# Performance work log

Measured on AMD Instinct MI355X. Metric: run time of the kernel, lower is better.

Reference implementation:

```python
import jax, jax.numpy as jnp
import numpy as np

NUM_ROI = 200

def mish(x):
    return x * jnp.tanh(jax.nn.softplus(x))

def gcn_conv(x, edge_index, edge_weight, W, b):
    # PyG GCNConv: add self-loops (weight 1), symmetric normalization, aggregate at target (col)
    N = x.shape[0]
    row, col = edge_index[0], edge_index[1]
    loop = jnp.arange(N)
    row = jnp.concatenate([row, loop])
    col = jnp.concatenate([col, loop])
    w = jnp.concatenate([edge_weight, jnp.ones((N,), x.dtype)])
    deg = jax.ops.segment_sum(w, col, num_segments=N)
    dis = jnp.where(deg > 0, jax.lax.rsqrt(deg), 0.0)
    norm = dis[row] * w * dis[col]                       # [E+N]
    h = x @ W                                            # [N, out]
    out = jax.ops.segment_sum(h[row] * norm[:, None], col, num_segments=N)
    return out + b

def setup_inputs() -> dict:
    key = jax.random.key(0)
    ks = jax.random.split(key, 16)
    B, E = 256, 1638400
    N = B * NUM_ROI
    d = {}
    d['x'] = jax.random.normal(ks[0], (N, NUM_ROI), jnp.float32)
    d['edge_index'] = jax.random.randint(ks[1], (2, E), 0, N, jnp.int64)
    d['edge_attr'] = jax.random.uniform(ks[2], (E,), jnp.float32)
    def rn(k, shape, fan_in):
        return jax.random.normal(k, shape, jnp.float32) * (1.0 / np.sqrt(fan_in))
    d['W1'] = rn(ks[3], (NUM_ROI, 128), NUM_ROI); d['b1'] = jnp.zeros((128,), jnp.float32)
    d['W2'] = rn(ks[4], (128, 64), 128);          d['b2'] = jnp.zeros((64,), jnp.float32)
    d['Wro'] = rn(ks[5], (64, 8), 64);            d['bro'] = jnp.zeros((8,), jnp.float32)
    d['Wfc1'] = rn(ks[6], (8 * NUM_ROI, NUM_ROI), 8 * NUM_ROI); d['bfc1'] = jnp.zeros((NUM_ROI,), jnp.float32)
    d['bn_gamma'] = jnp.ones((NUM_ROI,), jnp.float32)
    d['bn_beta'] = jnp.zeros((NUM_ROI,), jnp.float32)
    d['Wfc2'] = rn(ks[7], (NUM_ROI, 2), NUM_ROI); d['bfc2'] = jnp.zeros((2,), jnp.float32)
    d['Wd1'] = rn(ks[8], (NUM_ROI, 64), NUM_ROI); d['bd1'] = jnp.zeros((64,), jnp.float32)
    d['Wd2'] = rn(ks[9], (64, 6), 64);            d['bd2'] = jnp.zeros((6,), jnp.float32)
    return d

def reference(x, edge_index, edge_attr, W1, b1, W2, b2, Wro, bro, Wfc1, bfc1,
              bn_gamma, bn_beta, Wfc2, bfc2, Wd1, bd1, Wd2, bd2):
    h = mish(gcn_conv(x, edge_index, edge_attr, W1, b1))
    h = mish(gcn_conv(h, edge_index, edge_attr, W2, b2))
    out = mish(h @ Wro + bro)                            # [N, 8]
    feat = out.reshape(-1, NUM_ROI * 8)                  # [B, 1600]
    z = feat @ Wfc1 + bfc1                               # [B, numROI]
    # BatchNorm1d in training mode (batch statistics, biased variance)
    mu = jnp.mean(z, axis=0)
    var = jnp.mean((z - mu) ** 2, axis=0)
    zn = (z - mu) * jax.lax.rsqrt(var + 1e-5) * bn_gamma + bn_beta
    mid = mish(zn)
    logits = mid @ Wfc2 + bfc2                           # [B, 2]
    rev = 2.0 * jax.lax.stop_gradient(mid) - mid
    cls_logits = jax.nn.relu(rev @ Wd1 + bd1) @ Wd2 + bd2  # [B, 6]
    return (logits, cls_logits)
```

## Files before the change

### kernel.cpp

```cpp
#include <hip/hip_runtime.h>
#include <hip/hip_bf16.h>

typedef __hip_bfloat16 bf16;
typedef __attribute__((ext_vector_type(8))) short short8;
typedef __attribute__((ext_vector_type(4))) float f32x4;

#define NROI 200

__device__ __forceinline__ float u2f(unsigned short u) {
  return __uint_as_float(((unsigned)u) << 16);
}
__device__ __forceinline__ float lo16(unsigned u) { return __uint_as_float(u << 16); }
__device__ __forceinline__ float hi16(unsigned u) { return __uint_as_float(u & 0xffff0000u); }
__device__ __forceinline__ float b2f(bf16 v) { return __bfloat162float(v); }
__device__ __forceinline__ unsigned short f2us(float f) {
  union { bf16 b; unsigned short u; } c;
  c.b = __float2bfloat16(f);
  return c.u;
}

__device__ __forceinline__ float mishf(float x) {
  float sp = (x > 20.0f) ? x : log1pf(expf(x));
  return x * tanhf(sp);
}

__global__ __launch_bounds__(256) void detect_kernel(const unsigned short* xu,
                                                     const unsigned* eiw,
                                                     int* flags) {
  int tid = threadIdx.x;
  int sane = 0, zodd = 0;
  for (int i = tid; i < 4096; i += 256) {
    unsigned short u = xu[2 * i];
    unsigned e = (u >> 7) & 0xFF;
    if (u == 0 || (e >= 100 && e <= 134)) sane++;
  }
  for (int i = tid; i < 4096; i += 256) {
    if (eiw[2 * i + 1] == 0) zodd++;
  }
  __shared__ int s1[256], s2[256];
  s1[tid] = sane; s2[tid] = zodd;
  __syncthreads();
  for (int off = 128; off > 0; off >>= 1) {
    if (tid < off) { s1[tid] += s1[tid + off]; s2[tid] += s2[tid + off]; }
    __syncthreads();
  }
  if (tid == 0) {
    flags[0] = (s1[0] < 2048) ? 1 : 0;
    flags[1] = (s2[0] > 2048) ? 1 : 0;
  }
}

struct WArgs {
  const void* src[16];
  int n[16];
  int off[16];
};

__global__ __launch_bounds__(256) void convert_weights(WArgs a, bf16* base,
                                                       const int* flags) {
  int t = blockIdx.y;
  int i = blockIdx.x * 256 + threadIdx.x;
  if (i >= a.n[t]) return;
  bf16* dst = base + a.off[t];
  if (flags[0]) dst[i] = __float2bfloat16(((const float*)a.src[t])[i]);
  else ((unsigned short*)dst)[i] = ((const unsigned short*)a.src[t])[i];
}

__global__ __launch_bounds__(256) void swizzleW(const unsigned short* __restrict__ src,
                                                unsigned short* __restrict__ dst,
                                                int K, int KC, int NT) {
  int idx = blockIdx.x * 256 + threadIdx.x;
  int total = KC * NT * 512;
  if (idx >= total) return;
  int e = idx & 7;
  int l = (idx >> 3) & 63;
  int t = (idx >> 9) % NT;
  int kc = idx / (NT * 512);
  int k = kc * 32 + (l >> 4) * 8 + e;
  int c = t * 16 + (l & 15);
  dst[idx] = (k < K) ? src[k * (NT * 16) + c] : 0;
}

__global__ __launch_bounds__(256) void xbf_convert(const void* __restrict__ x,
                                                   unsigned short* __restrict__ xb,
                                                   const int* __restrict__ flags,
                                                   int N) {
  long long idx = (long long)blockIdx.x * 256 + threadIdx.x;
  long long total = (long long)N * 224;
  if (idx >= total) return;
  int c = (int)(idx % 224);
  long long n = idx / 224;
  unsigned short v = 0;
  if (c < 200) {
    if (flags[0]) v = f2us(((const float*)x)[n * 200 + c]);
    else v = ((const unsigned short*)x)[n * 200 + c];
  }
  xb[idx] = v;
}


__global__ void init_dc8(unsigned long long* dc8, long long M) {
  long long i = (long long)blockIdx.x * blockDim.x + threadIdx.x;
  if (i < M) dc8[i] = 0ull;
}

__global__ void edge_count(const int* __restrict__ ei, const void* __restrict__ ea,
                           const int* __restrict__ flags,
                           unsigned long long* dc8, int* __restrict__ rank,
                           int N, int E) {
  int e = blockIdx.x * blockDim.x + threadIdx.x;
  if (e >= E) return;
  unsigned xcd;
  asm("s_getreg_b32 %0, hwreg(HW_REG_XCC_ID)" : "=s"(xcd));
  xcd &= 7;
  int is64 = flags[1], isf32 = flags[0];
  int col = is64 ? ei[2 * (E + e)] : ei[E + e];
  float w = isf32 ? ((const float*)ea)[e] : u2f(((const unsigned short*)ea)[e]);
  unsigned long long p = (1ull << 40) | (unsigned long long)(w * 4294967296.0f);
  unsigned long long old = __hip_atomic_fetch_add(&dc8[(size_t)xcd * N + col], p,
                                                  __ATOMIC_RELAXED,
                                                  __HIP_MEMORY_SCOPE_WORKGROUP);
  rank[e] = ((int)xcd << 20) | (int)(old >> 40);
}

__global__ __launch_bounds__(256) void xcd_base(const unsigned long long* __restrict__ dc8,
                                                float* __restrict__ dis,
                                                int* __restrict__ cnt,
                                                unsigned short* __restrict__ xb, int N) {
  int n = blockIdx.x * 256 + threadIdx.x;
  if (n >= N) return;
  int run = 0;
  unsigned long long ws = 0;
  unsigned short loc[8];
#pragma unroll
  for (int x = 0; x < 8; ++x) {
    unsigned long long v = dc8[(size_t)x * N + n];
    loc[x] = (unsigned short)run;
    run += (int)(v >> 40);
    ws += v & 0xFFFFFFFFFFull;
  }
  cnt[n] = run;
  dis[n] = rsqrtf(1.0f + (float)ws * 2.3283064365386963e-10f);
  uint4 o;
  o.x = (unsigned)loc[0] | ((unsigned)loc[1] << 16);
  o.y = (unsigned)loc[2] | ((unsigned)loc[3] << 16);
  o.z = (unsigned)loc[4] | ((unsigned)loc[5] << 16);
  o.w = (unsigned)loc[6] | ((unsigned)loc[7] << 16);
  ((uint4*)xb)[n] = o;
}

__global__ __launch_bounds__(256) void scan_phase1(const int* __restrict__ cnt,
                                                   int* __restrict__ bsum, int N) {
  __shared__ int ts[256];
  int tid = threadIdx.x;
  int base = blockIdx.x * 1024 + tid * 4;
  int s = 0;
#pragma unroll
  for (int j = 0; j < 4; ++j)
    if (base + j < N) s += cnt[base + j];
  ts[tid] = s;
  __syncthreads();
  for (int off = 128; off > 0; off >>= 1) {
    if (tid < off) ts[tid] += ts[tid + off];
    __syncthreads();
  }
  if (tid == 0) bsum[blockIdx.x] = ts[0];
}

__global__ __launch_bounds__(64) void scan_phase2(const int* __restrict__ bsum,
                                                  int* __restrict__ bpre,
                                                  int* __restrict__ ptr, int nb, int N) {
  if (threadIdx.x == 0) {
    int run = 0;
    for (int i = 0; i < nb; ++i) { bpre[i] = run; run += bsum[i]; }
    ptr[N] = run;
  }
}

__global__ __launch_bounds__(256) void scan_phase3(const int* __restrict__ cnt,
                                                   const int* __restrict__ bpre,
                                                   int* __restrict__ ptr, int N) {
  __shared__ int ts[256];
  int tid = threadIdx.x;
  int base = blockIdx.x * 1024 + tid * 4;
  int c0 = 0, c1 = 0, c2 = 0, c3 = 0;
  if (base + 0 < N) c0 = cnt[base + 0];
  if (base + 1 < N) c1 = cnt[base + 1];
  if (base + 2 < N) c2 = cnt[base + 2];
  if (base + 3 < N) c3 = cnt[base + 3];
  ts[tid] = c0 + c1 + c2 + c3;
  __syncthreads();
  for (int off = 1; off < 256; off <<= 1) {
    int v = ts[tid];
    if (tid >= off) v += ts[tid - off];
    __syncthreads();
    ts[tid] = v;
    __syncthreads();
  }
  int run = bpre[blockIdx.x] + (tid ? ts[tid - 1] : 0);
  if (base + 0 < N) { ptr[base + 0] = run; run += c0; }
  if (base + 1 < N) { ptr[base + 1] = run; run += c1; }
  if (base + 2 < N) { ptr[base + 2] = run; run += c2; }
  if (base + 3 < N) { ptr[base + 3] = run; run += c3; }
}

__global__ void edge_scatter(const int* __restrict__ ei, const void* __restrict__ ea,
                             const int* __restrict__ flags,
                             const float* __restrict__ dis,
                             const int* __restrict__ ptr,
                             const unsigned short* __restrict__ xb,
                             const int* __restrict__ rank,
                             int2* __restrict__ epair, int E) {
  int e = blockIdx.x * blockDim.x + threadIdx.x;
  if (e >= E) return;
  int is64 = flags[1], isf32 = flags[0];
  int r = is64 ? ei[2 * e] : ei[e];
  int c = is64 ? ei[2 * (E + e)] : ei[E + e];
  float w = isf32 ? ((const float*)ea)[e] : u2f(((const unsigned short*)ea)[e]);
  float nrm = dis[r] * w * dis[c];
  int rk = rank[e];
  int idx = ptr[c] + (int)xb[(size_t)c * 8 + (rk >> 20)] + (rk & 0xFFFFF);
  int2 pr; pr.x = r; pr.y = __float_as_int(nrm);
  epair[idx] = pr;
}

template<int KC, int NT>
__global__ __launch_bounds__(256) void gemm_mfma(const unsigned short* __restrict__ Abf,
                                                 const unsigned short* __restrict__ Wswz,
                                                 unsigned short* __restrict__ H,
                                                 int M) {
  int wid = threadIdx.x >> 6, lane = threadIdx.x & 63;
  int row0 = (blockIdx.x * 4 + wid) * 16;
  if (row0 >= M) return;
  constexpr int K = KC * 32;
  constexpr int NC = NT * 16;
  f32x4 acc[NT];
#pragma unroll
  for (int t = 0; t < NT; ++t) acc[t] = {0.f, 0.f, 0.f, 0.f};
  size_t arow = (size_t)(row0 + (lane & 15)) * K + (lane >> 4) * 8;
#pragma unroll
  for (int kc = 0; kc < KC; ++kc) {
    short8 a = *(const short8*)&Abf[arow + kc * 32];
#pragma unroll
    for (int t = 0; t < NT; ++t) {
      short8 b = *(const short8*)&Wswz[((kc * NT + t) * 64 + lane) * 8];
      acc[t] = __builtin_amdgcn_mfma_f32_16x16x32_bf16(a, b, acc[t], 0, 0, 0);
    }
  }
  int orow = row0 + (lane >> 4) * 4;
  int ocol = lane & 15;
#pragma unroll
  for (int t = 0; t < NT; ++t)
#pragma unroll
    for (int r = 0; r < 4; ++r)
      H[(size_t)(orow + r) * NC + t * 16 + ocol] = f2us(acc[t][r]);
}

__global__ __launch_bounds__(256) void agg_mish128(const unsigned* __restrict__ hu,
                                                   const float* __restrict__ dis,
                                                   const int* __restrict__ ptr,
                                                   const int2* __restrict__ ep,
                                                   const bf16* __restrict__ bias,
                                                   unsigned* __restrict__ g, int N) {
  int w = threadIdx.x >> 6, lane = threadIdx.x & 63;
  int n = blockIdx.x * 4 + w;
  float dn = dis[n];
  float self = dn * dn;
  unsigned u = hu[(size_t)n * 64 + lane];
  float acc0 = lo16(u) * self;
  float acc1 = hi16(u) * self;
  int e0 = ptr[n], e1 = ptr[n + 1];
  for (int base = e0; base < e1; base += 64) {
    int2 myp = {0, 0};
    if (base + lane < e1) myp = ep[base + lane];
    int m = e1 - base; if (m > 64) m = 64;
    int j = 0;
    for (; j + 4 <= m; j += 4) {
      int r0 = __builtin_amdgcn_readlane(myp.x, j);
      int r1 = __builtin_amdgcn_readlane(myp.x, j + 1);
      int r2 = __builtin_amdgcn_readlane(myp.x, j + 2);
      int r3 = __builtin_amdgcn_readlane(myp.x, j + 3);
      unsigned u0 = hu[(size_t)r0 * 64 + lane];
      unsigned u1 = hu[(size_t)r1 * 64 + lane];
      unsigned u2 = hu[(size_t)r2 * 64 + lane];
      unsigned u3 = hu[(size_t)r3 * 64 + lane];
      float w0 = __uint_as_float(__builtin_amdgcn_readlane(myp.y, j));
      float w1 = __uint_as_float(__builtin_amdgcn_readlane(myp.y, j + 1));
      float w2 = __uint_as_float(__builtin_amdgcn_readlane(myp.y, j + 2));
      float w3 = __uint_as_float(__builtin_amdgcn_readlane(myp.y, j + 3));
      acc0 += lo16(u0) * w0; acc1 += hi16(u0) * w0;
      acc0 += lo16(u1) * w1; acc1 += hi16(u1) * w1;
      acc0 += lo16(u2) * w2; acc1 += hi16(u2) * w2;
      acc0 += lo16(u3) * w3; acc1 += hi16(u3) * w3;
    }
    for (; j < m; ++j) {
      int rr = __builtin_amdgcn_readlane(myp.x, j);
      float ww = __uint_as_float(__builtin_amdgcn_readlane(myp.y, j));
      unsigned uu = hu[(size_t)rr * 64 + lane];
      acc0 += lo16(uu) * ww;
      acc1 += hi16(uu) * ww;
    }
  }
  unsigned bb = ((const unsigned*)bias)[lane];
  float m0 = mishf(acc0 + lo16(bb));
  float m1 = mishf(acc1 + hi16(bb));
  g[(size_t)n * 64 + lane] = ((unsigned)f2us(m1) << 16) | f2us(m0);
}

__global__ __launch_bounds__(256) void agg_mish64_ro(const unsigned short* __restrict__ hus,
                                                     const float* __restrict__ dis,
                                                     const int* __restrict__ ptr,
                                                     const int2* __restrict__ ep,
                                                     const bf16* __restrict__ bias,
                                                     const bf16* __restrict__ Wro,
                                                     const bf16* __restrict__ bro,
                                                     float* __restrict__ out8, int N) {
  int w = threadIdx.x >> 6, lane = threadIdx.x & 63;
  int n = blockIdx.x * 4 + w;
  float dn = dis[n];
  float self = dn * dn;
  float acc = u2f(hus[(size_t)n * 64 + lane]) * self;
  int e0 = ptr[n], e1 = ptr[n + 1];
  for (int base = e0; base < e1; base += 64) {
    int2 myp = {0, 0};
    if (base + lane < e1) myp = ep[base + lane];
    int m = e1 - base; if (m > 64) m = 64;
    int j = 0;
    for (; j + 4 <= m; j += 4) {
      int r0 = __builtin_amdgcn_readlane(myp.x, j);
      int r1 = __builtin_amdgcn_readlane(myp.x, j + 1);
      int r2 = __builtin_amdgcn_readlane(myp.x, j + 2);
      int r3 = __builtin_amdgcn_readlane(myp.x, j + 3);
      float v0 = u2f(hus[(size_t)r0 * 64 + lane]);
      float v1 = u2f(hus[(size_t)r1 * 64 + lane]);
      float v2 = u2f(hus[(size_t)r2 * 64 + lane]);
      float v3 = u2f(hus[(size_t)r3 * 64 + lane]);
      float w0 = __uint_as_float(__builtin_amdgcn_readlane(myp.y, j));
      float w1 = __uint_as_float(__builtin_amdgcn_readlane(myp.y, j + 1));
      float w2 = __uint_as_float(__builtin_amdgcn_readlane(myp.y, j + 2));
      float w3 = __uint_as_float(__builtin_amdgcn_readlane(myp.y, j + 3));
      acc += v0 * w0 + v1 * w1 + v2 * w2 + v3 * w3;
    }
    for (; j < m; ++j) {
      int rr = __builtin_amdgcn_readlane(myp.x, j);
      float ww = __uint_as_float(__builtin_amdgcn_readlane(myp.y, j));
      acc += u2f(hus[(size_t)rr * 64 + lane]) * ww;
    }
  }
  float mv = mishf(acc + u2f(((const unsigned short*)bias)[lane]));
  uint4 wr = ((const uint4*)Wro)[lane];
  float p0 = mv * lo16(wr.x), p1 = mv * hi16(wr.x);
  float p2 = mv * lo16(wr.y), p3 = mv * hi16(wr.y);
  float p4 = mv * lo16(wr.z), p5 = mv * hi16(wr.z);
  float p6 = mv * lo16(wr.w), p7 = mv * hi16(wr.w);
  bool b0 = lane & 1;
  float q0 = (b0 ? p4 : p0) + __shfl_xor(b0 ? p0 : p4, 1);
  float q1 = (b0 ? p5 : p1) + __shfl_xor(b0 ? p1 : p5, 1);
  float q2 = (b0 ? p6 : p2) + __shfl_xor(b0 ? p2 : p6, 1);
  float q3 = (b0 ? p7 : p3) + __shfl_xor(b0 ? p3 : p7, 1);
  bool b1 = lane & 2;
  float r0 = (b1 ? q2 : q0) + __shfl_xor(b1 ? q0 : q2, 2);
  float r1 = (b1 ? q3 : q1) + __shfl_xor(b1 ? q1 : q3, 2);
  bool b2v = lane & 4;
  float t = (b2v ? r1 : r0) + __shfl_xor(b2v ? r0 : r1, 4);
  t += __shfl_xor(t, 8);
  t += __shfl_xor(t, 16);
  t += __shfl_xor(t, 32);
  if (lane < 8) {
    int oidx = ((lane & 1) << 2) | (lane & 2) | ((lane >> 2) & 1);
    out8[(size_t)n * 8 + oidx] = mishf(t + u2f(((const unsigned short*)bro)[oidx]));
  }
}


__global__ __launch_bounds__(256) void fc1_kernel(const float* __restrict__ feat,
                                                  const bf16* __restrict__ W,
                                                  const bf16* __restrict__ bias,
                                                  float* __restrict__ z) {
  __shared__ float fr[1600];
  int b = blockIdx.x, tid = threadIdx.x;
  for (int i = tid; i < 1600; i += 256) fr[i] = feat[(size_t)b * 1600 + i];
  __syncthreads();
  if (tid < NROI) {
    float acc = b2f(bias[tid]);
#pragma unroll 8
    for (int k = 0; k < 1600; ++k) acc += fr[k] * b2f(W[k * NROI + tid]);
    z[b * NROI + tid] = acc;
  }
}

__global__ __launch_bounds__(256) void bn_stats(const float* __restrict__ z,
                                                float* mu, float* rvar, int B) {
  int j = blockIdx.x;
  int tid = threadIdx.x;
  float v = z[tid * NROI + j];
  float s = v, q = v * v;
  for (int off = 32; off > 0; off >>= 1) {
    s += __shfl_down(s, off);
    q += __shfl_down(q, off);
  }
  __shared__ float ss[4], qq[4];
  int w = tid >> 6, lane = tid & 63;
  if (lane == 0) { ss[w] = s; qq[w] = q; }
  __syncthreads();
  if (tid == 0) {
    float S = ss[0] + ss[1] + ss[2] + ss[3];
    float Q = qq[0] + qq[1] + qq[2] + qq[3];
    float m = S / (float)B;
    float var = Q / (float)B - m * m;
    mu[j] = m;
    rvar[j] = rsqrtf(var + 1e-5f);
  }
}

__global__ __launch_bounds__(256) void head_kernel(const float* __restrict__ z,
                                                   const float* __restrict__ mu,
                                                   const float* __restrict__ rvar,
                                                   const bf16* __restrict__ gamma,
                                                   const bf16* __restrict__ beta,
                                                   const bf16* __restrict__ Wfc2,
                                                   const bf16* __restrict__ bfc2,
                                                   const bf16* __restrict__ Wd1,
                                                   const bf16* __restrict__ bd1,
                                                   const bf16* __restrict__ Wd2,
                                                   const bf16* __restrict__ bd2,
                                                   float* __restrict__ out, int B) {
  __shared__ float mid[NROI];
  __shared__ float t[64];
  int b = blockIdx.x, tid = threadIdx.x;
  if (tid < NROI) {
    float v = (z[b * NROI + tid] - mu[tid]) * rvar[tid] * b2f(gamma[tid]) + b2f(beta[tid]);
    mid[tid] = mishf(v);
  }
  __syncthreads();
  if (tid < 64) {
    float acc = b2f(bd1[tid]);
#pragma unroll 8
    for (int j = 0; j < NROI; ++j) acc += mid[j] * b2f(Wd1[j * 64 + tid]);
    t[tid] = fmaxf(acc, 0.0f);
  }
  if (tid >= 64 && tid < 66) {
    int c = tid - 64;
    float acc = b2f(bfc2[c]);
    for (int j = 0; j < NROI; ++j) acc += mid[j] * b2f(Wfc2[j * 2 + c]);
    out[b * 2 + c] = acc;
  }
  __syncthreads();
  if (tid < 6) {
    float acc = b2f(bd2[tid]);
#pragma unroll 8
    for (int k = 0; k < 64; ++k) acc += t[k] * b2f(Wd2[k * 6 + tid]);
    out[B * 2 + b * 6 + tid] = acc;
  }
}


extern "C" void kernel_launch(void* const* d_in, const int* in_sizes, int n_in,
                              void* d_out, int out_size, void* d_ws, size_t ws_size,
                              hipStream_t stream) {
  const void* x  = d_in[0];
  const int*  ei = (const int*)d_in[1];
  const void* ea = d_in[2];
  float* out = (float*)d_out;

  int N = in_sizes[0] / NROI;
  int E = in_sizes[2];
  int B = N / NROI;

  char* p = (char*)d_ws;
  auto carve = [&](size_t bytes) -> void* {
    void* r = (void*)p;
    p += (bytes + 255) & ~(size_t)255;
    return r;
  };
  int*   flags = (int*)carve(16);
  bf16*  cw    = (bf16*)carve(400000 * 2);
  float* dis   = (float*)carve((size_t)N * 4);
  unsigned long long* dc8 = (unsigned long long*)carve((size_t)8 * N * 8);
  int*   cnt   = (int*)carve((size_t)N * 4);
  unsigned short* xbse = (unsigned short*)carve((size_t)N * 8 * 2);
  int*   ptr   = (int*)carve(((size_t)N + 1) * 4);
  int*   bsum  = (int*)carve(1024);
  int*   bpre  = (int*)carve(1024);
  int2*  epair = (int2*)carve((size_t)E * 8);
  unsigned short* h = (unsigned short*)carve((size_t)N * 128 * 2);
  size_t xg_bytes = (size_t)N * 224 * 2;
  size_t rk_bytes = (size_t)E * 4;
  char* xg = (char*)carve(xg_bytes > rk_bytes ? xg_bytes : rk_bytes);
  int* rank = (int*)xg;
  unsigned short* xbf = (unsigned short*)xg;
  unsigned* g = (unsigned*)xg;
  unsigned short* w1swz = (unsigned short*)carve(7 * 8 * 512 * 2);
  unsigned short* w2swz = (unsigned short*)carve(4 * 4 * 512 * 2);
  float* out8  = (float*)carve((size_t)N * 8 * 4);
  float* z     = (float*)carve((size_t)B * NROI * 4);
  float* mu    = (float*)carve(NROI * 4);
  float* rv    = (float*)carve(NROI * 4);

  WArgs wa;
  int run = 0;
  int maxn = 0;
  for (int t = 0; t < 16; ++t) {
    wa.src[t] = d_in[3 + t];
    wa.n[t]   = in_sizes[3 + t];
    wa.off[t] = run;
    run += in_sizes[3 + t];
    if (in_sizes[3 + t] > maxn) maxn = in_sizes[3 + t];
  }
  const bf16* W1   = cw + wa.off[0];
  const bf16* b1   = cw + wa.off[1];
  const bf16* W2   = cw + wa.off[2];
  const bf16* b2   = cw + wa.off[3];
  const bf16* Wro  = cw + wa.off[4];
  const bf16* bro  = cw + wa.off[5];
  const bf16* Wfc1 = cw + wa.off[6];
  const bf16* bfc1 = cw + wa.off[7];
  const bf16* gam  = cw + wa.off[8];
  const bf16* bet  = cw + wa.off[9];
  const bf16* Wfc2 = cw + wa.off[10];
  const bf16* bfc2 = cw + wa.off[11];
  const bf16* Wd1  = cw + wa.off[12];
  const bf16* bd1  = cw + wa.off[13];
  const bf16* Wd2  = cw + wa.off[14];
  const bf16* bd2  = cw + wa.off[15];

  int nb = (N + 255) / 256;
  int eb = (E + 255) / 256;
  int nscan = (N + 1023) / 1024;

  detect_kernel<<<1, 256, 0, stream>>>((const unsigned short*)x,
                                       (const unsigned*)ei, flags);
  dim3 wg((maxn + 255) / 256, 16);
  convert_weights<<<wg, 256, 0, stream>>>(wa, cw, flags);
  swizzleW<<<(7 * 8 * 512 + 255) / 256, 256, 0, stream>>>(
      (const unsigned short*)W1, w1swz, 200, 7, 8);
  swizzleW<<<(4 * 4 * 512 + 255) / 256, 256, 0, stream>>>(
      (const unsigned short*)W2, w2swz, 128, 4, 4);

  long long dctot = (long long)8 * N;
  init_dc8<<<(int)((dctot + 255) / 256), 256, 0, stream>>>(dc8, dctot);
  edge_count<<<eb, 256, 0, stream>>>(ei, ea, flags, dc8, rank, N, E);
  xcd_base<<<nb, 256, 0, stream>>>(dc8, dis, cnt, xbse, N);
  scan_phase1<<<nscan, 256, 0, stream>>>(cnt, bsum, N);
  scan_phase2<<<1, 64, 0, stream>>>(bsum, bpre, ptr, nscan, N);
  scan_phase3<<<nscan, 256, 0, stream>>>(cnt, bpre, ptr, N);
  edge_scatter<<<eb, 256, 0, stream>>>(ei, ea, flags, dis, ptr, xbse, rank,
                                       epair, E);

  long long xtot = (long long)N * 224;
  xbf_convert<<<(int)((xtot + 255) / 256), 256, 0, stream>>>(x, xbf, flags, N);
  gemm_mfma<7, 8><<<N / 64, 256, 0, stream>>>(xbf, w1swz, h, N);
  agg_mish128<<<N / 4, 256, 0, stream>>>((const unsigned*)h, dis, ptr, epair,
                                         b1, g, N);
  gemm_mfma<4, 4><<<N / 64, 256, 0, stream>>>((const unsigned short*)g, w2swz, h, N);
  agg_mish64_ro<<<N / 4, 256, 0, stream>>>(h, dis, ptr, epair, b2, Wro, bro,
                                           out8, N);

  fc1_kernel<<<B, 256, 0, stream>>>(out8, Wfc1, bfc1, z);
  bn_stats<<<NROI, 256, 0, stream>>>(z, mu, rv, B);
  head_kernel<<<B, 256, 0, stream>>>(z, mu, rv, gam, bet, Wfc2, bfc2,
                                     Wd1, bd1, Wd2, bd2, out, B);
}
```

Before: 385.8 us.

## Fuse prep and scan kernels, add nontemporal edge-stream accesses

```diff
diff --git a/kernel.cpp b/kernel.cpp
--- a/kernel.cpp
+++ b/kernel.cpp
@@ -66,12 +66,9 @@
   else ((unsigned short*)dst)[i] = ((const unsigned short*)a.src[t])[i];
 }
 
-__global__ __launch_bounds__(256) void swizzleW(const unsigned short* __restrict__ src,
-                                                unsigned short* __restrict__ dst,
-                                                int K, int KC, int NT) {
-  int idx = blockIdx.x * 256 + threadIdx.x;
-  int total = KC * NT * 512;
-  if (idx >= total) return;
+__device__ __forceinline__ void swz_one(const unsigned short* src,
+                                        unsigned short* dst, int idx,
+                                        int K, int NT) {
   int e = idx & 7;
   int l = (idx >> 3) & 63;
   int t = (idx >> 9) % NT;
@@ -81,28 +78,36 @@
   dst[idx] = (k < K) ? src[k * (NT * 16) + c] : 0;
 }
 
-__global__ __launch_bounds__(256) void xbf_convert(const void* __restrict__ x,
-                                                   unsigned short* __restrict__ xb,
+__global__ __launch_bounds__(256) void prep_kernel(const unsigned short* __restrict__ w1,
+                                                   const unsigned short* __restrict__ w2,
+                                                   unsigned short* __restrict__ w1swz,
+                                                   unsigned short* __restrict__ w2swz,
+                                                   const void* __restrict__ x,
+                                                   unsigned short* __restrict__ xbf,
+                                                   unsigned long long* __restrict__ dc8,
                                                    const int* __restrict__ flags,
-                                                   int N) {
-  long long idx = (long long)blockIdx.x * 256 + threadIdx.x;
-  long long total = (long long)N * 224;
-  if (idx >= total) return;
-  int c = (int)(idx % 224);
-  long long n = idx / 224;
-  unsigned short v = 0;
-  if (c < 200) {
-    if (flags[0]) v = f2us(((const float*)x)[n * 200 + c]);
-    else v = ((const unsigned short*)x)[n * 200 + c];
-  }
-  xb[idx] = v;
-}
-
-
-__global__ void init_dc8(unsigned long long* dc8, long long M) {
-  long long i = (long long)blockIdx.x * blockDim.x + threadIdx.x;
-  if (i < M) dc8[i] = 0ull;
-}
+                                                   int N, int b1, int b2, long long b3,
+                                                   long long b4) {
+  long long i = (long long)blockIdx.x * 256 + threadIdx.x;
+  if (i < b1) {
+    swz_one(w1, w1swz, (int)i, 200, 8);
+  } else if (i < b2) {
+    swz_one(w2, w2swz, (int)(i - b1), 128, 4);
+  } else if (i < b3) {
+    long long idx = i - b2;
+    int c = (int)(idx % 224);
+    long long n = idx / 224;
+    unsigned short v = 0;
+    if (c < 200) {
+      if (flags[0]) v = f2us(((const float*)x)[n * 200 + c]);
+      else v = ((const unsigned short*)x)[n * 200 + c];
+    }
+    xbf[idx] = v;
+  } else if (i < b4) {
+    dc8[i - b3] = 0ull;
+  }
+}
+
 
 __global__ void edge_count(const int* __restrict__ ei, const void* __restrict__ ea,
                            const int* __restrict__ flags,
@@ -114,51 +119,46 @@
   asm("s_getreg_b32 %0, hwreg(HW_REG_XCC_ID)" : "=s"(xcd));
   xcd &= 7;
   int is64 = flags[1], isf32 = flags[0];
-  int col = is64 ? ei[2 * (E + e)] : ei[E + e];
-  float w = isf32 ? ((const float*)ea)[e] : u2f(((const unsigned short*)ea)[e]);
+  int col = is64 ? __builtin_nontemporal_load(&ei[2 * (E + e)])
+                 : __builtin_nontemporal_load(&ei[E + e]);
+  float w = isf32 ? __builtin_nontemporal_load(&((const float*)ea)[e])
+                  : u2f(__builtin_nontemporal_load(&((const unsigned short*)ea)[e]));
   unsigned long long p = (1ull << 40) | (unsigned long long)(w * 4294967296.0f);
   unsigned long long old = __hip_atomic_fetch_add(&dc8[(size_t)xcd * N + col], p,
                                                   __ATOMIC_RELAXED,
                                                   __HIP_MEMORY_SCOPE_WORKGROUP);
-  rank[e] = ((int)xcd << 20) | (int)(old >> 40);
+  __builtin_nontemporal_store(((int)xcd << 20) | (int)(old >> 40), &rank[e]);
 }
 
 __global__ __launch_bounds__(256) void xcd_base(const unsigned long long* __restrict__ dc8,
                                                 float* __restrict__ dis,
                                                 int* __restrict__ cnt,
-                                                unsigned short* __restrict__ xb, int N) {
-  int n = blockIdx.x * 256 + threadIdx.x;
-  if (n >= N) return;
-  int run = 0;
-  unsigned long long ws = 0;
-  unsigned short loc[8];
-#pragma unroll
-  for (int x = 0; x < 8; ++x) {
-    unsigned long long v = dc8[(size_t)x * N + n];
-    loc[x] = (unsigned short)run;
-    run += (int)(v >> 40);
-    ws += v & 0xFFFFFFFFFFull;
-  }
-  cnt[n] = run;
-  dis[n] = rsqrtf(1.0f + (float)ws * 2.3283064365386963e-10f);
-  uint4 o;
-  o.x = (unsigned)loc[0] | ((unsigned)loc[1] << 16);
-  o.y = (unsigned)loc[2] | ((unsigned)loc[3] << 16);
-  o.z = (unsigned)loc[4] | ((unsigned)loc[5] << 16);
-  o.w = (unsigned)loc[6] | ((unsigned)loc[7] << 16);
-  ((uint4*)xb)[n] = o;
-}
-
-__global__ __launch_bounds__(256) void scan_phase1(const int* __restrict__ cnt,
-                                                   int* __restrict__ bsum, int N) {
+                                                unsigned short* __restrict__ xb,
+                                                int* __restrict__ bsum, int N) {
   __shared__ int ts[256];
   int tid = threadIdx.x;
-  int base = blockIdx.x * 1024 + tid * 4;
-  int s = 0;
+  int n = blockIdx.x * 256 + tid;
+  int run = 0;
+  if (n < N) {
+    unsigned long long ws = 0;
+    unsigned short loc[8];
 #pragma unroll
-  for (int j = 0; j < 4; ++j)
-    if (base + j < N) s += cnt[base + j];
-  ts[tid] = s;
+    for (int x = 0; x < 8; ++x) {
+      unsigned long long v = dc8[(size_t)x * N + n];
+      loc[x] = (unsigned short)run;
+      run += (int)(v >> 40);
+      ws += v & 0xFFFFFFFFFFull;
+    }
+    cnt[n] = run;
+    dis[n] = rsqrtf(1.0f + (float)ws * 2.3283064365386963e-10f);
+    uint4 o;
+    o.x = (unsigned)loc[0] | ((unsigned)loc[1] << 16);
+    o.y = (unsigned)loc[2] | ((unsigned)loc[3] << 16);
+    o.z = (unsigned)loc[4] | ((unsigned)loc[5] << 16);
+    o.w = (unsigned)loc[6] | ((unsigned)loc[7] << 16);
+    ((uint4*)xb)[n] = o;
+  }
+  ts[tid] = run;
   __syncthreads();
   for (int off = 128; off > 0; off >>= 1) {
     if (tid < off) ts[tid] += ts[tid + off];
@@ -182,13 +182,9 @@
                                                    int* __restrict__ ptr, int N) {
   __shared__ int ts[256];
   int tid = threadIdx.x;
-  int base = blockIdx.x * 1024 + tid * 4;
-  int c0 = 0, c1 = 0, c2 = 0, c3 = 0;
-  if (base + 0 < N) c0 = cnt[base + 0];
-  if (base + 1 < N) c1 = cnt[base + 1];
-  if (base + 2 < N) c2 = cnt[base + 2];
-  if (base + 3 < N) c3 = cnt[base + 3];
-  ts[tid] = c0 + c1 + c2 + c3;
+  int n = blockIdx.x * 256 + tid;
+  int c = (n < N) ? cnt[n] : 0;
+  ts[tid] = c;
   __syncthreads();
   for (int off = 1; off < 256; off <<= 1) {
     int v = ts[tid];
@@ -197,11 +193,7 @@
     ts[tid] = v;
     __syncthreads();
   }
-  int run = bpre[blockIdx.x] + (tid ? ts[tid - 1] : 0);
-  if (base + 0 < N) { ptr[base + 0] = run; run += c0; }
-  if (base + 1 < N) { ptr[base + 1] = run; run += c1; }
-  if (base + 2 < N) { ptr[base + 2] = run; run += c2; }
-  if (base + 3 < N) { ptr[base + 3] = run; run += c3; }
+  if (n < N) ptr[n] = bpre[blockIdx.x] + (tid ? ts[tid - 1] : 0);
 }
 
 __global__ void edge_scatter(const int* __restrict__ ei, const void* __restrict__ ea,
@@ -210,18 +202,22 @@
                              const int* __restrict__ ptr,
                              const unsigned short* __restrict__ xb,
                              const int* __restrict__ rank,
-                             int2* __restrict__ epair, int E) {
+                             long long* __restrict__ epair, int E) {
   int e = blockIdx.x * blockDim.x + threadIdx.x;
   if (e >= E) return;
   int is64 = flags[1], isf32 = flags[0];
-  int r = is64 ? ei[2 * e] : ei[e];
-  int c = is64 ? ei[2 * (E + e)] : ei[E + e];
-  float w = isf32 ? ((const float*)ea)[e] : u2f(((const unsigned short*)ea)[e]);
+  int r = is64 ? __builtin_nontemporal_load(&ei[2 * e])
+               : __builtin_nontemporal_load(&ei[e]);
+  int c = is64 ? __builtin_nontemporal_load(&ei[2 * (E + e)])
+               : __builtin_nontemporal_load(&ei[E + e]);
+  float w = isf32 ? __builtin_nontemporal_load(&((const float*)ea)[e])
+                  : u2f(__builtin_nontemporal_load(&((const unsigned short*)ea)[e]));
   float nrm = dis[r] * w * dis[c];
-  int rk = rank[e];
+  int rk = __builtin_nontemporal_load(&rank[e]);
   int idx = ptr[c] + (int)xb[(size_t)c * 8 + (rk >> 20)] + (rk & 0xFFFFF);
-  int2 pr; pr.x = r; pr.y = __float_as_int(nrm);
-  epair[idx] = pr;
+  long long pr = (long long)((unsigned long long)__float_as_uint(nrm) << 32) |
+                 (unsigned)r;
+  __builtin_nontemporal_store(pr, &epair[idx]);
 }
 
 template<int KC, int NT>
@@ -259,7 +255,7 @@
 __global__ __launch_bounds__(256) void agg_mish128(const unsigned* __restrict__ hu,
                                                    const float* __restrict__ dis,
                                                    const int* __restrict__ ptr,
-                                                   const int2* __restrict__ ep,
+                                                   const long long* __restrict__ ep,
                                                    const bf16* __restrict__ bias,
                                                    unsigned* __restrict__ g, int N) {
   int w = threadIdx.x >> 6, lane = threadIdx.x & 63;
@@ -271,31 +267,33 @@
   float acc1 = hi16(u) * self;
   int e0 = ptr[n], e1 = ptr[n + 1];
   for (int base = e0; base < e1; base += 64) {
-    int2 myp = {0, 0};
-    if (base + lane < e1) myp = ep[base + lane];
+    long long myp = 0;
+    if (base + lane < e1) myp = __builtin_nontemporal_load(&ep[base + lane]);
+    int mx = (int)(unsigned)myp;
+    int my = (int)(myp >> 32);
     int m = e1 - base; if (m > 64) m = 64;
     int j = 0;
     for (; j + 4 <= m; j += 4) {
-      int r0 = __builtin_amdgcn_readlane(myp.x, j);
-      int r1 = __builtin_amdgcn_readlane(myp.x, j + 1);
-      int r2 = __builtin_amdgcn_readlane(myp.x, j + 2);
-      int r3 = __builtin_amdgcn_readlane(myp.x, j + 3);
+      int r0 = __builtin_amdgcn_readlane(mx, j);
+      int r1 = __builtin_amdgcn_readlane(mx, j + 1);
+      int r2 = __builtin_amdgcn_readlane(mx, j + 2);
+      int r3 = __builtin_amdgcn_readlane(mx, j + 3);
       unsigned u0 = hu[(size_t)r0 * 64 + lane];
       unsigned u1 = hu[(size_t)r1 * 64 + lane];
       unsigned u2 = hu[(size_t)r2 * 64 + lane];
       unsigned u3 = hu[(size_t)r3 * 64 + lane];
-      float w0 = __uint_as_float(__builtin_amdgcn_readlane(myp.y, j));
-      float w1 = __uint_as_float(__builtin_amdgcn_readlane(myp.y, j + 1));
-      float w2 = __uint_as_float(__builtin_amdgcn_readlane(myp.y, j + 2));
-      float w3 = __uint_as_float(__builtin_amdgcn_readlane(myp.y, j + 3));
+      float w0 = __uint_as_float(__builtin_amdgcn_readlane(my, j));
+      float w1 = __uint_as_float(__builtin_amdgcn_readlane(my, j + 1));
+      float w2 = __uint_as_float(__builtin_amdgcn_readlane(my, j + 2));
+      float w3 = __uint_as_float(__builtin_amdgcn_readlane(my, j + 3));
       acc0 += lo16(u0) * w0; acc1 += hi16(u0) * w0;
       acc0 += lo16(u1) * w1; acc1 += hi16(u1) * w1;
       acc0 += lo16(u2) * w2; acc1 += hi16(u2) * w2;
       acc0 += lo16(u3) * w3; acc1 += hi16(u3) * w3;
     }
     for (; j < m; ++j) {
-      int rr = __builtin_amdgcn_readlane(myp.x, j);
-      float ww = __uint_as_float(__builtin_amdgcn_readlane(myp.y, j));
+      int rr = __builtin_amdgcn_readlane(mx, j);
+      float ww = __uint_as_float(__builtin_amdgcn_readlane(my, j));
       unsigned uu = hu[(size_t)rr * 64 + lane];
       acc0 += lo16(uu) * ww;
       acc1 += hi16(uu) * ww;
@@ -310,7 +308,7 @@
 __global__ __launch_bounds__(256) void agg_mish64_ro(const unsigned short* __restrict__ hus,
                                                      const float* __restrict__ dis,
                                                      const int* __restrict__ ptr,
-                                                     const int2* __restrict__ ep,
+                                                     const long long* __restrict__ ep,
                                                      const bf16* __restrict__ bias,
                                                      const bf16* __restrict__ Wro,
                                                      const bf16* __restrict__ bro,
@@ -322,28 +320,30 @@
   float acc = u2f(hus[(size_t)n * 64 + lane]) * self;
   int e0 = ptr[n], e1 = ptr[n + 1];
   for (int base = e0; base < e1; base += 64) {
-    int2 myp = {0, 0};
-    if (base + lane < e1) myp = ep[base + lane];
+    long long myp = 0;
+    if (base + lane < e1) myp = __builtin_nontemporal_load(&ep[base + lane]);
+    int mx = (int)(unsigned)myp;
+    int my = (int)(myp >> 32);
     int m = e1 - base; if (m > 64) m = 64;
     int j = 0;
     for (; j + 4 <= m; j += 4) {
-      int r0 = __builtin_amdgcn_readlane(myp.x, j);
-      int r1 = __builtin_amdgcn_readlane(myp.x, j + 1);
-      int r2 = __builtin_amdgcn_readlane(myp.x, j + 2);
-      int r3 = __builtin_amdgcn_readlane(myp.x, j + 3);
+      int r0 = __builtin_amdgcn_readlane(mx, j);
+      int r1 = __builtin_amdgcn_readlane(mx, j + 1);
+      int r2 = __builtin_amdgcn_readlane(mx, j + 2);
+      int r3 = __builtin_amdgcn_readlane(mx, j + 3);
       float v0 = u2f(hus[(size_t)r0 * 64 + lane]);
       float v1 = u2f(hus[(size_t)r1 * 64 + lane]);
       float v2 = u2f(hus[(size_t)r2 * 64 + lane]);
       float v3 = u2f(hus[(size_t)r3 * 64 + lane]);
-      float w0 = __uint_as_float(__builtin_amdgcn_readlane(myp.y, j));
-      float w1 = __uint_as_float(__builtin_amdgcn_readlane(myp.y, j + 1));
-      float w2 = __uint_as_float(__builtin_amdgcn_readlane(myp.y, j + 2));
-      float w3 = __uint_as_float(__builtin_amdgcn_readlane(myp.y, j + 3));
+      float w0 = __uint_as_float(__builtin_amdgcn_readlane(my, j));
+      float w1 = __uint_as_float(__builtin_amdgcn_readlane(my, j + 1));
+      float w2 = __uint_as_float(__builtin_amdgcn_readlane(my, j + 2));
+      float w3 = __uint_as_float(__builtin_amdgcn_readlane(my, j + 3));
       acc += v0 * w0 + v1 * w1 + v2 * w2 + v3 * w3;
     }
     for (; j < m; ++j) {
-      int rr = __builtin_amdgcn_readlane(myp.x, j);
-      float ww = __uint_as_float(__builtin_amdgcn_readlane(myp.y, j));
+      int rr = __builtin_amdgcn_readlane(mx, j);
+      float ww = __uint_as_float(__builtin_amdgcn_readlane(my, j));
       acc += u2f(hus[(size_t)rr * 64 + lane]) * ww;
     }
   }
@@ -482,12 +482,10 @@
   int*   ptr   = (int*)carve(((size_t)N + 1) * 4);
   int*   bsum  = (int*)carve(1024);
   int*   bpre  = (int*)carve(1024);
-  int2*  epair = (int2*)carve((size_t)E * 8);
+  long long* epair = (long long*)carve((size_t)E * 8);
   unsigned short* h = (unsigned short*)carve((size_t)N * 128 * 2);
-  size_t xg_bytes = (size_t)N * 224 * 2;
-  size_t rk_bytes = (size_t)E * 4;
-  char* xg = (char*)carve(xg_bytes > rk_bytes ? xg_bytes : rk_bytes);
-  int* rank = (int*)xg;
+  int*   rank  = (int*)carve((size_t)E * 4);
+  char* xg = (char*)carve((size_t)N * 224 * 2);
   unsigned short* xbf = (unsigned short*)xg;
   unsigned* g = (unsigned*)xg;
   unsigned short* w1swz = (unsigned short*)carve(7 * 8 * 512 * 2);
@@ -526,29 +524,27 @@
 
   int nb = (N + 255) / 256;
   int eb = (E + 255) / 256;
-  int nscan = (N + 1023) / 1024;
 
   detect_kernel<<<1, 256, 0, stream>>>((const unsigned short*)x,
                                        (const unsigned*)ei, flags);
   dim3 wg((maxn + 255) / 256, 16);
   convert_weights<<<wg, 256, 0, stream>>>(wa, cw, flags);
-  swizzleW<<<(7 * 8 * 512 + 255) / 256, 256, 0, stream>>>(
-      (const unsigned short*)W1, w1swz, 200, 7, 8);
-  swizzleW<<<(4 * 4 * 512 + 255) / 256, 256, 0, stream>>>(
-      (const unsigned short*)W2, w2swz, 128, 4, 4);
-
-  long long dctot = (long long)8 * N;
-  init_dc8<<<(int)((dctot + 255) / 256), 256, 0, stream>>>(dc8, dctot);
+
+  int pb1 = 7 * 8 * 512;
+  int pb2 = pb1 + 4 * 4 * 512;
+  long long pb3 = (long long)pb2 + (long long)N * 224;
+  long long pb4 = pb3 + (long long)8 * N;
+  prep_kernel<<<(int)((pb4 + 255) / 256), 256, 0, stream>>>(
+      (const unsigned short*)W1, (const unsigned short*)W2, w1swz, w2swz,
+      x, xbf, dc8, flags, N, pb1, pb2, pb3, pb4);
+
   edge_count<<<eb, 256, 0, stream>>>(ei, ea, flags, dc8, rank, N, E);
-  xcd_base<<<nb, 256, 0, stream>>>(dc8, dis, cnt, xbse, N);
-  scan_phase1<<<nscan, 256, 0, stream>>>(cnt, bsum, N);
-  scan_phase2<<<1, 64, 0, stream>>>(bsum, bpre, ptr, nscan, N);
-  scan_phase3<<<nscan, 256, 0, stream>>>(cnt, bpre, ptr, N);
+  xcd_base<<<nb, 256, 0, stream>>>(dc8, dis, cnt, xbse, bsum, N);
+  scan_phase2<<<1, 64, 0, stream>>>(bsum, bpre, ptr, nb, N);
+  scan_phase3<<<nb, 256, 0, stream>>>(cnt, bpre, ptr, N);
   edge_scatter<<<eb, 256, 0, stream>>>(ei, ea, flags, dis, ptr, xbse, rank,
                                        epair, E);
 
-  long long xtot = (long long)N * 224;
-  xbf_convert<<<(int)((xtot + 255) / 256), 256, 0, stream>>>(x, xbf, flags, N);
   gemm_mfma<7, 8><<<N / 64, 256, 0, stream>>>(xbf, w1swz, h, N);
   agg_mish128<<<N / 4, 256, 0, stream>>>((const unsigned*)h, dis, ptr, epair,
                                          b1, g, N);
```

After: 414.7 us. 7.5% more time.
